# Performance work log

Measured on AMD Instinct MI355X. Metric: run time of the kernel, lower is better.

The kernel has to match this reference:

```python
import jax, jax.numpy as jnp
import numpy as np

N = 50000   # nodes
E = 800000  # edges per layer
D = 128     # feature dim
H = 256     # mlp hidden
O = 3       # output dim


def setup_inputs() -> dict:
    key = jax.random.key(0)
    ks = jax.random.split(key, 16)
    def lin(k, fan_out, fan_in):
        s = 1.0 / np.sqrt(fan_in)
        kw, kb = jax.random.split(k)
        return (jax.random.uniform(kw, (fan_out, fan_in), jnp.float32, -s, s),
                jax.random.uniform(kb, (fan_out,), jnp.float32, -s, s))
    x = jax.random.normal(ks[0], (N, D), jnp.float32)
    edge_idx0 = jax.random.randint(ks[1], (2, E), 0, N, dtype=jnp.int64)
    edge_idx1 = jax.random.randint(ks[2], (2, E), 0, N, dtype=jnp.int64)
    Wl1, bl1 = lin(ks[3], D, D)   # SAGE layer1: lin_l (aggregated neighbors, with bias)
    Wr1, _ = lin(ks[4], D, D)     # SAGE layer1: lin_r (root, no bias)
    Wl2, bl2 = lin(ks[5], D, D)
    Wr2, _ = lin(ks[6], D, D)
    Ws, bs = lin(ks[7], D, D)     # skip_fc
    W1, b1 = lin(ks[8], H, D)     # mlp hidden
    W2, b2 = lin(ks[9], O, H)     # mlp out
    return dict(x=x, edge_idx0=edge_idx0, edge_idx1=edge_idx1,
                Wl1=Wl1, bl1=bl1, Wr1=Wr1, Wl2=Wl2, bl2=bl2, Wr2=Wr2,
                Ws=Ws, bs=bs, W1=W1, b1=b1, W2=W2, b2=b2)


def _sage(x, ei, Wl, bl, Wr):
    # PyG SAGEConv with mean aggregation: out = lin_l(mean_j x_j) + lin_r(x_i)
    src, dst = ei[0], ei[1]
    agg = jax.ops.segment_sum(x[src], dst, num_segments=N)          # [N, D] gather-scatter
    cnt = jax.ops.segment_sum(jnp.ones((ei.shape[1],), x.dtype), dst, num_segments=N)
    agg = agg / jnp.maximum(cnt, 1.0)[:, None]
    return agg @ Wl.T + bl + x @ Wr.T


def reference(x, edge_idx0, edge_idx1, Wl1, bl1, Wr1, Wl2, bl2, Wr2,
              Ws, bs, W1, b1, W2, b2):
    inp = x
    h = _sage(x, edge_idx0, Wl1, bl1, Wr1)
    h = _sage(h, edge_idx1, Wl2, bl2, Wr2)
    h = h + (inp @ Ws.T + bs)            # skip connection
    h = jax.nn.relu(h @ W1.T + b1)       # MLP head
    return h @ W2.T + b2                  # [N, 3]
```

## Files before the change

### kernel.cpp

```cpp
#include <hip/hip_runtime.h>
#include <hip/hip_bf16.h>


#define DD 128
#define SB 8
#define CH 4096
typedef unsigned short u16;
typedef __attribute__((ext_vector_type(8))) short short8;
typedef __attribute__((ext_vector_type(4))) float f32x4;

__device__ inline u16 f2bf(float f) {
    __hip_bfloat16 h = __float2bfloat16(f);
    u16 u;
    __builtin_memcpy(&u, &h, 2);
    return u;
}
__device__ inline unsigned pack2(float lo, float hi) {
    return (unsigned)f2bf(lo) | ((unsigned)f2bf(hi) << 16);
}
__device__ inline float bf_lo(unsigned u) { union { unsigned x; float f; } c; c.x = u << 16; return c.f; }
__device__ inline float bf_hi(unsigned u) { union { unsigned x; float f; } c; c.x = u & 0xffff0000u; return c.f; }

struct CastJobs {
    const float4* src[6];
    uint2* dst[6];
    int qstart[7];
};
__global__ __launch_bounds__(256) void cast_kernel(CastJobs jb) {
    int q = blockIdx.x * 256 + threadIdx.x;
    if (q >= jb.qstart[6]) return;
    int i = 0;
#pragma unroll
    for (int k = 1; k < 6; ++k) if (q >= jb.qstart[k]) i = k;
    int local = q - jb.qstart[i];
    float4 v = jb.src[i][local];
    jb.dst[i][local] = make_uint2(pack2(v.x, v.y), pack2(v.z, v.w));
}

__global__ __launch_bounds__(256) void hist1_kernel(const int* __restrict__ dst0, int* __restrict__ h0,
                                                    const int* __restrict__ dst1, int* __restrict__ h1,
                                                    int e0, int e1, int nb, int P) {
    int arr = blockIdx.y;
    const int* dst = arr ? dst1 : dst0;
    int* hist = arr ? h1 : h0;
    int e = arr ? e1 : e0;
    __shared__ int h[256];
    int t = threadIdx.x;
    h[t] = 0;
    __syncthreads();
    int base = blockIdx.x * CH;
    int hi = min(base + CH, e);
    for (int i = base + t; i < hi; i += 256) atomicAdd(&h[dst[i] >> SB], 1);
    __syncthreads();
    if (t < nb) hist[t * P + blockIdx.x] = h[t];
}

__global__ __launch_bounds__(256) void rowsum_kernel(const int* __restrict__ h0, int* __restrict__ bs0,
                                                     const int* __restrict__ h1, int* __restrict__ bs1,
                                                     int P) {
    int arr = blockIdx.y;
    const int* hist = arr ? h1 : h0;
    int* bs = arr ? bs1 : bs0;
    int b = blockIdx.x;
    __shared__ int s[256];
    int t = threadIdx.x;
    s[t] = (t < P) ? hist[b * P + t] : 0;
    __syncthreads();
    for (int off = 128; off; off >>= 1) {
        if (t < off) s[t] += s[t + off];
        __syncthreads();
    }
    if (t == 0) bs[b] = s[0];
}

__global__ __launch_bounds__(256) void bscan_kernel(const int* __restrict__ bs0, int* __restrict__ bb0, int* __restrict__ rp0, int e0,
                                                    const int* __restrict__ bs1, int* __restrict__ bb1, int* __restrict__ rp1, int e1,
                                                    int nb, int n) {
    int arr = blockIdx.x;
    const int* bsum = arr ? bs1 : bs0;
    int* bb = arr ? bb1 : bb0;
    int* rp = arr ? rp1 : rp0;
    int E = arr ? e1 : e0;
    __shared__ int s[256];
    int t = threadIdx.x;
    int v = (t < nb) ? bsum[t] : 0;
    s[t] = v;
    __syncthreads();
    for (int off = 1; off < 256; off <<= 1) {
        int u = (t >= off) ? s[t - off] : 0;
        __syncthreads();
        s[t] += u;
        __syncthreads();
    }
    if (t < nb) bb[t] = s[t] - v;
    if (t == 0) { bb[nb] = E; rp[n] = E; }
}

__global__ __launch_bounds__(256) void offs_kernel(int* __restrict__ h0, const int* __restrict__ bb0,
                                                   int* __restrict__ h1, const int* __restrict__ bb1,
                                                   int P) {
    int arr = blockIdx.y;
    int* hist = arr ? h1 : h0;
    const int* bb = arr ? bb1 : bb0;
    int b = blockIdx.x;
    __shared__ int s[256];
    int t = threadIdx.x;
    int v = (t < P) ? hist[b * P + t] : 0;
    s[t] = v;
    __syncthreads();
    for (int off = 1; off < 256; off <<= 1) {
        int u = (t >= off) ? s[t - off] : 0;
        __syncthreads();
        s[t] += u;
        __syncthreads();
    }
    if (t < P) hist[b * P + t] = s[t] - v + bb[b];
}

__global__ __launch_bounds__(256) void scatter1_kernel(
    const int* __restrict__ src0, const int* __restrict__ dst0, const int* __restrict__ h0, unsigned* __restrict__ binned0,
    const int* __restrict__ src1, const int* __restrict__ dst1, const int* __restrict__ h1, unsigned* __restrict__ binned1,
    int e0, int e1, int nb, int P) {
    int arr = blockIdx.y;
    const int* src = arr ? src1 : src0;
    const int* dst = arr ? dst1 : dst0;
    const int* hist = arr ? h1 : h0;
    unsigned* binned = arr ? binned1 : binned0;
    int e = arr ? e1 : e0;
    int p = blockIdx.x;
    __shared__ int cnt[256];
    int t = threadIdx.x;
    if (t < nb) cnt[t] = hist[t * P + p];
    __syncthreads();
    int base = p * CH;
    int hi = min(base + CH, e);
    for (int i = base + t; i < hi; i += 256) {
        int d = dst[i];
        int pos = atomicAdd(&cnt[d >> SB], 1);
        binned[pos] = ((unsigned)d << 16) | (unsigned)src[i];
    }
}

__global__ __launch_bounds__(256) void place_kernel(
    const unsigned* __restrict__ binned0, const int* __restrict__ bb0, int* __restrict__ rp0, u16* __restrict__ csr0,
    const unsigned* __restrict__ binned1, const int* __restrict__ bb1, int* __restrict__ rp1, u16* __restrict__ csr1,
    int n, int nb) {
    int arr = blockIdx.y;
    const unsigned* binned = arr ? binned1 : binned0;
    const int* bb = arr ? bb1 : bb0;
    int* rp = arr ? rp1 : rp0;
    u16* csr = arr ? csr1 : csr0;
    int b = blockIdx.x;
    __shared__ int cnt[256];
    __shared__ int s[256];
    int t = threadIdx.x;
    int base = bb[b], end = bb[b + 1];
    cnt[t] = 0;
    __syncthreads();
    for (int i = base + t; i < end; i += 256)
        atomicAdd(&cnt[(binned[i] >> 16) & 255], 1);
    __syncthreads();
    int deg = cnt[t];
    s[t] = deg;
    __syncthreads();
    for (int off = 1; off < 256; off <<= 1) {
        int u = (t >= off) ? s[t - off] : 0;
        __syncthreads();
        s[t] += u;
        __syncthreads();
    }
    int gpos = base + s[t] - deg;
    int node = (b << SB) + t;
    if (node < n) rp[node] = gpos;
    cnt[t] = gpos;
    __syncthreads();
    for (int i = base + t; i < end; i += 256) {
        unsigned pk = binned[i];
        int ld = (pk >> 16) & 255;
        int pos = atomicAdd(&cnt[ld], 1);
        csr[pos] = (u16)(pk & 0xffffu);
    }
}

__global__ __launch_bounds__(256) void agg1_kernel(const unsigned* __restrict__ G1L,
                                                   const unsigned* __restrict__ G1M,
                                                   const u16* __restrict__ csr,
                                                   const int* __restrict__ rp,
                                                   const float* __restrict__ bl1,
                                                   unsigned* __restrict__ h1, int n) {
    int g = (blockIdx.x * 256 + threadIdx.x) >> 6;
    int lane = threadIdx.x & 63;
    if (g >= n) return;
    int start = rp[g], end = rp[g + 1];
    float a0 = 0.f, a1 = 0.f;
    int e = start;
    for (; e + 7 < end; e += 8) {
        int s0 = csr[e],     s1 = csr[e + 1], s2 = csr[e + 2], s3 = csr[e + 3];
        int s4 = csr[e + 4], s5 = csr[e + 5], s6 = csr[e + 6], s7 = csr[e + 7];
        unsigned v0 = G1L[(size_t)s0 * 64 + lane];
        unsigned v1 = G1L[(size_t)s1 * 64 + lane];
        unsigned v2 = G1L[(size_t)s2 * 64 + lane];
        unsigned v3 = G1L[(size_t)s3 * 64 + lane];
        unsigned v4 = G1L[(size_t)s4 * 64 + lane];
        unsigned v5 = G1L[(size_t)s5 * 64 + lane];
        unsigned v6 = G1L[(size_t)s6 * 64 + lane];
        unsigned v7 = G1L[(size_t)s7 * 64 + lane];
        a0 += ((bf_lo(v0) + bf_lo(v1)) + (bf_lo(v2) + bf_lo(v3))) +
              ((bf_lo(v4) + bf_lo(v5)) + (bf_lo(v6) + bf_lo(v7)));
        a1 += ((bf_hi(v0) + bf_hi(v1)) + (bf_hi(v2) + bf_hi(v3))) +
              ((bf_hi(v4) + bf_hi(v5)) + (bf_hi(v6) + bf_hi(v7)));
    }
    for (; e + 3 < end; e += 4) {
        int s0 = csr[e], s1 = csr[e + 1], s2 = csr[e + 2], s3 = csr[e + 3];
        unsigned v0 = G1L[(size_t)s0 * 64 + lane];
        unsigned v1 = G1L[(size_t)s1 * 64 + lane];
        unsigned v2 = G1L[(size_t)s2 * 64 + lane];
        unsigned v3 = G1L[(size_t)s3 * 64 + lane];
        a0 += (bf_lo(v0) + bf_lo(v1)) + (bf_lo(v2) + bf_lo(v3));
        a1 += (bf_hi(v0) + bf_hi(v1)) + (bf_hi(v2) + bf_hi(v3));
    }
    for (; e < end; ++e) {
        unsigned v0 = G1L[(size_t)csr[e] * 64 + lane];
        a0 += bf_lo(v0);
        a1 += bf_hi(v0);
    }
    float sc = 1.0f / (float)max(end - start, 1);
    unsigned m = G1M[(size_t)g * 64 + lane];
    float2 b = ((const float2*)bl1)[lane];
    h1[(size_t)g * 64 + lane] = pack2(a0 * sc + bf_lo(m) + b.x, a1 * sc + bf_hi(m) + b.y);
}

__global__ __launch_bounds__(256) void agg2_kernel(const unsigned* __restrict__ G2L,
                                                   const unsigned* __restrict__ G2R,
                                                   const unsigned* __restrict__ G1R,
                                                   const u16* __restrict__ csr,
                                                   const int* __restrict__ rp,
                                                   const float* __restrict__ bl2,
                                                   const float* __restrict__ bs,
                                                   unsigned* __restrict__ h3, int n) {
    int g = (blockIdx.x * 256 + threadIdx.x) >> 6;
    int lane = threadIdx.x & 63;
    if (g >= n) return;
    int start = rp[g], end = rp[g + 1];
    float a0 = 0.f, a1 = 0.f;
    int e = start;
    for (; e + 7 < end; e += 8) {
        int s0 = csr[e],     s1 = csr[e + 1], s2 = csr[e + 2], s3 = csr[e + 3];
        int s4 = csr[e + 4], s5 = csr[e + 5], s6 = csr[e + 6], s7 = csr[e + 7];
        unsigned v0 = G2L[(size_t)s0 * 64 + lane];
        unsigned v1 = G2L[(size_t)s1 * 64 + lane];
        unsigned v2 = G2L[(size_t)s2 * 64 + lane];
        unsigned v3 = G2L[(size_t)s3 * 64 + lane];
        unsigned v4 = G2L[(size_t)s4 * 64 + lane];
        unsigned v5 = G2L[(size_t)s5 * 64 + lane];
        unsigned v6 = G2L[(size_t)s6 * 64 + lane];
        unsigned v7 = G2L[(size_t)s7 * 64 + lane];
        a0 += ((bf_lo(v0) + bf_lo(v1)) + (bf_lo(v2) + bf_lo(v3))) +
              ((bf_lo(v4) + bf_lo(v5)) + (bf_lo(v6) + bf_lo(v7)));
        a1 += ((bf_hi(v0) + bf_hi(v1)) + (bf_hi(v2) + bf_hi(v3))) +
              ((bf_hi(v4) + bf_hi(v5)) + (bf_hi(v6) + bf_hi(v7)));
    }
    for (; e + 3 < end; e += 4) {
        int s0 = csr[e], s1 = csr[e + 1], s2 = csr[e + 2], s3 = csr[e + 3];
        unsigned v0 = G2L[(size_t)s0 * 64 + lane];
        unsigned v1 = G2L[(size_t)s1 * 64 + lane];
        unsigned v2 = G2L[(size_t)s2 * 64 + lane];
        unsigned v3 = G2L[(size_t)s3 * 64 + lane];
        a0 += (bf_lo(v0) + bf_lo(v1)) + (bf_lo(v2) + bf_lo(v3));
        a1 += (bf_hi(v0) + bf_hi(v1)) + (bf_hi(v2) + bf_hi(v3));
    }
    for (; e < end; ++e) {
        unsigned v0 = G2L[(size_t)csr[e] * 64 + lane];
        a0 += bf_lo(v0);
        a1 += bf_hi(v0);
    }
    float sc = 1.0f / (float)max(end - start, 1);
    unsigned m2 = G2R[(size_t)g * 64 + lane];
    unsigned m1 = G1R[(size_t)g * 64 + lane];
    float2 b = ((const float2*)bl2)[lane];
    float2 s2 = ((const float2*)bs)[lane];
    h3[(size_t)g * 64 + lane] = pack2(a0 * sc + bf_lo(m2) + bf_lo(m1) + b.x + s2.x,
                                      a1 * sc + bf_hi(m2) + bf_hi(m1) + b.y + s2.y);
}

__device__ inline void load_af_f32(const void* Av, int rowA, int half, short8* af) {
    const float4* Arow = (const float4*)Av + (size_t)rowA * 32 + half * 2;
#pragma unroll
    for (int kk = 0; kk < 4; ++kk) {
        float4 a = Arow[kk * 8], b = Arow[kk * 8 + 1];
        uint4 v = make_uint4(pack2(a.x, a.y), pack2(a.z, a.w),
                             pack2(b.x, b.y), pack2(b.z, b.w));
        af[kk] = *(short8*)&v;
    }
}
__device__ inline void load_af_bf16(const void* Av, int rowA, int half, short8* af) {
    const uint4* Arow = (const uint4*)Av + (size_t)rowA * 16 + half;
#pragma unroll
    for (int kk = 0; kk < 4; ++kk) {
        uint4 v = Arow[kk * 4];
        af[kk] = *(short8*)&v;
    }
}

template <bool F32A>
__global__ __launch_bounds__(256) void mfma_gemm(const void* __restrict__ Av,
                                                 const u16* __restrict__ W,
                                                 u16* __restrict__ C, int M) {
    __shared__ u16 Bs[32 * 512];
    const int t = threadIdx.x;
    const int colBase = blockIdx.y * 128;
    u16* Cp = C + (size_t)blockIdx.y * M * 128;
    const int w = t >> 6, lane = t & 63, r = lane & 15, half = lane >> 4;
    const int nTiles = M >> 4;
    const int stride = gridDim.x * 4;
    int tile = blockIdx.x * 4 + w;

    short8 af[4];
    if (tile < nTiles) {
        if (F32A) load_af_f32(Av, (tile << 4) + r, half, af);
        else      load_af_bf16(Av, (tile << 4) + r, half, af);
    }
#pragma unroll
    for (int i = 0; i < 8; ++i) {
        int id = t + 256 * i;
        int nrow = id >> 4, cc = id & 15;
        int f = ((nrow >> 4) << 2) | (cc >> 2);
        int dl = ((cc & 3) << 4) | (nrow & 15);
        *(uint4*)&Bs[(f * 64 + dl) * 8] = ((const uint4*)W)[(size_t)(colBase + nrow) * 16 + cc];
    }
    __syncthreads();
    const u16* bB = &Bs[lane * 8];
    for (; tile < nTiles; tile += stride) {
        int nextTile = tile + stride;
        short8 afn[4];
        if (nextTile < nTiles) {
            if (F32A) load_af_f32(Av, (nextTile << 4) + r, half, afn);
            else      load_af_bf16(Av, (nextTile << 4) + r, half, afn);
        }
        f32x4 acc[8];
#pragma unroll
        for (int i = 0; i < 8; ++i) acc[i] = (f32x4){0.f, 0.f, 0.f, 0.f};
#pragma unroll
        for (int kk = 0; kk < 4; ++kk)
#pragma unroll
            for (int ct = 0; ct < 8; ++ct) {
                short8 bf = *(const short8*)(bB + (ct * 4 + kk) * 512);
                acc[ct] = __builtin_amdgcn_mfma_f32_16x16x32_bf16(af[kk], bf, acc[ct], 0, 0, 0);
            }
#pragma unroll
        for (int ct = 0; ct < 8; ++ct) {
            int col = ct * 16 + r;
#pragma unroll
            for (int reg = 0; reg < 4; ++reg) {
                int row = (tile << 4) + half * 4 + reg;
                Cp[(size_t)row * 128 + col] = f2bf(acc[ct][reg]);
            }
        }
#pragma unroll
        for (int kk = 0; kk < 4; ++kk) af[kk] = afn[kk];
    }
}

__global__ __launch_bounds__(256) void gemm_out_kernel(const u16* __restrict__ h3,
                                                       const u16* __restrict__ W1,
                                                       const float* __restrict__ b1,
                                                       const float* __restrict__ W2,
                                                       const float* __restrict__ b2,
                                                       float* __restrict__ out, int M) {
    __shared__ u16 Bs[64 * 512];
    __shared__ float w2s[3 * 256];
    __shared__ float b1s[256];
    const int t = threadIdx.x;
    const int w = t >> 6, lane = t & 63, r = lane & 15, half = lane >> 4;
    const int nTiles = M >> 4;
    const int stride = gridDim.x * 4;
    int tile = blockIdx.x * 4 + w;

    short8 af[4];
    if (tile < nTiles) load_af_bf16(h3, (tile << 4) + r, half, af);
#pragma unroll
    for (int i = 0; i < 16; ++i) {
        int id = t + 256 * i;
        int nrow = id >> 4, cc = id & 15;
        int f = ((nrow >> 4) << 2) | (cc >> 2);
        int dl = ((cc & 3) << 4) | (nrow & 15);
        *(uint4*)&Bs[(f * 64 + dl) * 8] = ((const uint4*)W1)[(size_t)nrow * 16 + cc];
    }
    for (int i = t; i < 768; i += 256) w2s[i] = W2[i];
    b1s[t] = b1[t];
    __syncthreads();
    const u16* bB = &Bs[lane * 8];
    float c0 = b2[0], c1 = b2[1], c2 = b2[2];
    for (; tile < nTiles; tile += stride) {
        int nextTile = tile + stride;
        short8 afn[4];
        if (nextTile < nTiles) load_af_bf16(h3, (nextTile << 4) + r, half, afn);
        f32x4 acc[16];
#pragma unroll
        for (int i = 0; i < 16; ++i) acc[i] = (f32x4){0.f, 0.f, 0.f, 0.f};
#pragma unroll
        for (int kk = 0; kk < 4; ++kk)
#pragma unroll
            for (int ct = 0; ct < 16; ++ct) {
                short8 bf = *(const short8*)(bB + (ct * 4 + kk) * 512);
                acc[ct] = __builtin_amdgcn_mfma_f32_16x16x32_bf16(af[kk], bf, acc[ct], 0, 0, 0);
            }
        float p[4][3] = {{0.f, 0.f, 0.f}, {0.f, 0.f, 0.f}, {0.f, 0.f, 0.f}, {0.f, 0.f, 0.f}};
#pragma unroll
        for (int ct = 0; ct < 16; ++ct) {
            int col = ct * 16 + r;
            float bv = b1s[col];
            float w0 = w2s[col], w1 = w2s[256 + col], w2v = w2s[512 + col];
#pragma unroll
            for (int reg = 0; reg < 4; ++reg) {
                float h4 = fmaxf(acc[ct][reg] + bv, 0.f);
                p[reg][0] += h4 * w0;
                p[reg][1] += h4 * w1;
                p[reg][2] += h4 * w2v;
            }
        }
#pragma unroll
        for (int m = 1; m < 16; m <<= 1)
#pragma unroll
            for (int reg = 0; reg < 4; ++reg) {
                p[reg][0] += __shfl_xor(p[reg][0], m);
                p[reg][1] += __shfl_xor(p[reg][1], m);
                p[reg][2] += __shfl_xor(p[reg][2], m);
            }
        if (r == 0) {
#pragma unroll
            for (int reg = 0; reg < 4; ++reg) {
                int row = (tile << 4) + half * 4 + reg;
                out[(size_t)row * 3 + 0] = p[reg][0] + c0;
                out[(size_t)row * 3 + 1] = p[reg][1] + c1;
                out[(size_t)row * 3 + 2] = p[reg][2] + c2;
            }
        }
#pragma unroll
        for (int kk = 0; kk < 4; ++kk) af[kk] = afn[kk];
    }
}

extern "C" void kernel_launch(void* const* d_in, const int* in_sizes, int n_in,
                              void* d_out, int out_size, void* d_ws, size_t ws_size,
                              hipStream_t stream) {
    const float* x   = (const float*)d_in[0];
    const int*   ei0 = (const int*)d_in[1];
    const int*   ei1 = (const int*)d_in[2];
    const float* Wl1 = (const float*)d_in[3];
    const float* bl1 = (const float*)d_in[4];
    const float* Wr1 = (const float*)d_in[5];
    const float* Wl2 = (const float*)d_in[6];
    const float* bl2 = (const float*)d_in[7];
    const float* Wr2 = (const float*)d_in[8];
    const float* Wsk = (const float*)d_in[9];
    const float* bsk = (const float*)d_in[10];
    const float* W1  = (const float*)d_in[11];
    const float* b1  = (const float*)d_in[12];
    const float* W2  = (const float*)d_in[13];
    const float* b2  = (const float*)d_in[14];
    float* out = (float*)d_out;

    const int N  = in_sizes[0] / DD;
    const int E0 = in_sizes[1] / 2;
    const int E1 = in_sizes[2] / 2;
    const int H  = in_sizes[12];

    const int* src0 = ei0;      const int* dst0 = ei0 + E0;
    const int* src1 = ei1;      const int* dst1 = ei1 + E1;

    const int nb   = (N + 255) >> SB;
    const int Emax = (E0 > E1) ? E0 : E1;
    const int P    = (Emax + CH - 1) / CH;

    char* wp = (char*)d_ws;
    auto carve = [&](size_t bytes) { char* p = wp; wp += (bytes + 255) & ~(size_t)255; return p; };
    u16* G1   = (u16*)carve((size_t)3 * N * DD * 2);
    u16* G2   = (u16*)carve((size_t)2 * N * DD * 2);
    u16* h1h  = (u16*)carve((size_t)N * DD * 2);
    u16* h3h  = (u16*)carve((size_t)N * DD * 2);
    u16* wc1  = (u16*)carve((size_t)384 * DD * 2);
    u16* wc2  = (u16*)carve((size_t)256 * DD * 2);
    u16* w1h  = (u16*)carve((size_t)H * DD * 2);
    int* rp0  = (int*)carve((size_t)(N + 1) * 4);
    int* rp1  = (int*)carve((size_t)(N + 1) * 4);
    u16* csr0 = (u16*)carve((size_t)E0 * 2);
    u16* csr1 = (u16*)carve((size_t)E1 * 2);
    unsigned* binned0 = (unsigned*)carve((size_t)E0 * 4);
    unsigned* binned1 = (unsigned*)carve((size_t)E1 * 4);
    int* hist1_0 = (int*)carve((size_t)nb * P * 4);
    int* hist1_1 = (int*)carve((size_t)nb * P * 4);
    int* bsum0 = (int*)carve((size_t)nb * 4);
    int* bsum1 = (int*)carve((size_t)nb * 4);
    int* bb0 = (int*)carve((size_t)(nb + 1) * 4);
    int* bb1 = (int*)carve((size_t)(nb + 1) * 4);

    const u16* G1L = G1;
    const u16* G1M = G1 + (size_t)N * DD;
    const u16* G1R = G1 + (size_t)2 * N * DD;
    const u16* G2L = G2;
    const u16* G2R = G2 + (size_t)N * DD;

    CastJobs jb;
    const float* srcs[6] = {Wl1, Wr1, Wsk, Wl2, Wr2, W1};
    u16* dsts[6] = {wc1, wc1 + 128 * DD, wc1 + 256 * DD, wc2, wc2 + 128 * DD, w1h};
    int  cnts[6] = {DD * DD, DD * DD, DD * DD, DD * DD, DD * DD, H * DD};
    int q = 0;
    for (int i = 0; i < 6; ++i) {
        jb.src[i] = (const float4*)srcs[i];
        jb.dst[i] = (uint2*)dsts[i];
        jb.qstart[i] = q;
        q += cnts[i] / 4;
    }
    jb.qstart[6] = q;

    const int gAgg = (N * 64 + 255) / 256;

    cast_kernel<<<(q + 255) / 256, 256, 0, stream>>>(jb);
    hist1_kernel<<<dim3(P, 2), 256, 0, stream>>>(dst0, hist1_0, dst1, hist1_1, E0, E1, nb, P);
    rowsum_kernel<<<dim3(nb, 2), 256, 0, stream>>>(hist1_0, bsum0, hist1_1, bsum1, P);
    bscan_kernel<<<2, 256, 0, stream>>>(bsum0, bb0, rp0, E0, bsum1, bb1, rp1, E1, nb, N);
    offs_kernel<<<dim3(nb, 2), 256, 0, stream>>>(hist1_0, bb0, hist1_1, bb1, P);
    scatter1_kernel<<<dim3(P, 2), 256, 0, stream>>>(src0, dst0, hist1_0, binned0,
                                                    src1, dst1, hist1_1, binned1, E0, E1, nb, P);
    place_kernel<<<dim3(nb, 2), 256, 0, stream>>>(binned0, bb0, rp0, csr0,
                                                  binned1, bb1, rp1, csr1, N, nb);

    mfma_gemm<true><<<dim3(320, 3), 256, 0, stream>>>(x, wc1, G1, N);
    agg1_kernel<<<gAgg, 256, 0, stream>>>((const unsigned*)G1L, (const unsigned*)G1M,
                                          csr0, rp0, bl1, (unsigned*)h1h, N);
    mfma_gemm<false><<<dim3(320, 2), 256, 0, stream>>>(h1h, wc2, G2, N);
    agg2_kernel<<<gAgg, 256, 0, stream>>>((const unsigned*)G2L, (const unsigned*)G2R,
                                          (const unsigned*)G1R, csr1, rp1, bl2, bsk,
                                          (unsigned*)h3h, N);
    gemm_out_kernel<<<512, 256, 0, stream>>>(h3h, w1h, b1, W2, b2, out, N);
}
```

Measured before the change: 261.4 us.

## Chunk neighbor features by column slice per XCD and fuse weight cast into GEMMs

The GEMM now writes the lin_l projection in four 32-column chunks stored contiguously per chunk. The aggregation kernels map block IDs so each pair of XCDs gathers only one chunk, keeping each XCD's gather working set (about 3.2MB) small enough to stay in its L2. Separately, the standalone weight-cast kernel is removed, and the GEMMs convert fp32 weights to bf16 while loading them into LDS. This trades one launch for redundant per-block conversion work. Each node's gather now uses 16 lanes, so more edge-index reads are repeated across chunks.

After: 285.9 us. +9.3%, slower.

```diff
diff --git a/kernel.cpp b/kernel.cpp
--- a/kernel.cpp
+++ b/kernel.cpp
@@ -20,22 +20,6 @@
 }
 __device__ inline float bf_lo(unsigned u) { union { unsigned x; float f; } c; c.x = u << 16; return c.f; }
 __device__ inline float bf_hi(unsigned u) { union { unsigned x; float f; } c; c.x = u & 0xffff0000u; return c.f; }
-
-struct CastJobs {
-    const float4* src[6];
-    uint2* dst[6];
-    int qstart[7];
-};
-__global__ __launch_bounds__(256) void cast_kernel(CastJobs jb) {
-    int q = blockIdx.x * 256 + threadIdx.x;
-    if (q >= jb.qstart[6]) return;
-    int i = 0;
-#pragma unroll
-    for (int k = 1; k < 6; ++k) if (q >= jb.qstart[k]) i = k;
-    int local = q - jb.qstart[i];
-    float4 v = jb.src[i][local];
-    jb.dst[i][local] = make_uint2(pack2(v.x, v.y), pack2(v.z, v.w));
-}
 
 __global__ __launch_bounds__(256) void hist1_kernel(const int* __restrict__ dst0, int* __restrict__ h0,
                                                     const int* __restrict__ dst1, int* __restrict__ h1,
@@ -182,55 +166,52 @@
     }
 }
 
-__global__ __launch_bounds__(256) void agg1_kernel(const unsigned* __restrict__ G1L,
+__global__ __launch_bounds__(256) void agg1_kernel(const unsigned* __restrict__ G1Lc,
                                                    const unsigned* __restrict__ G1M,
                                                    const u16* __restrict__ csr,
                                                    const int* __restrict__ rp,
                                                    const float* __restrict__ bl1,
                                                    unsigned* __restrict__ h1, int n) {
-    int g = (blockIdx.x * 256 + threadIdx.x) >> 6;
-    int lane = threadIdx.x & 63;
+    int xcd = blockIdx.x & 7;
+    int chunk = xcd >> 1;
+    int nodeBlock = (blockIdx.x >> 3) * 2 + (xcd & 1);
+    int w = threadIdx.x >> 6, lane = threadIdx.x & 63;
+    int g = nodeBlock * 16 + w * 4 + (lane >> 4);
+    int c = lane & 15;
     if (g >= n) return;
+    const unsigned* base = G1Lc + (size_t)chunk * n * 16;
     int start = rp[g], end = rp[g + 1];
     float a0 = 0.f, a1 = 0.f;
     int e = start;
     for (; e + 7 < end; e += 8) {
         int s0 = csr[e],     s1 = csr[e + 1], s2 = csr[e + 2], s3 = csr[e + 3];
         int s4 = csr[e + 4], s5 = csr[e + 5], s6 = csr[e + 6], s7 = csr[e + 7];
-        unsigned v0 = G1L[(size_t)s0 * 64 + lane];
-        unsigned v1 = G1L[(size_t)s1 * 64 + lane];
-        unsigned v2 = G1L[(size_t)s2 * 64 + lane];
-        unsigned v3 = G1L[(size_t)s3 * 64 + lane];
-        unsigned v4 = G1L[(size_t)s4 * 64 + lane];
-        unsigned v5 = G1L[(size_t)s5 * 64 + lane];
-        unsigned v6 = G1L[(size_t)s6 * 64 + lane];
-        unsigned v7 = G1L[(size_t)s7 * 64 + lane];
+        unsigned v0 = base[(size_t)s0 * 16 + c];
+        unsigned v1 = base[(size_t)s1 * 16 + c];
+        unsigned v2 = base[(size_t)s2 * 16 + c];
+        unsigned v3 = base[(size_t)s3 * 16 + c];
+        unsigned v4 = base[(size_t)s4 * 16 + c];
+        unsigned v5 = base[(size_t)s5 * 16 + c];
+        unsigned v6 = base[(size_t)s6 * 16 + c];
+        unsigned v7 = base[(size_t)s7 * 16 + c];
         a0 += ((bf_lo(v0) + bf_lo(v1)) + (bf_lo(v2) + bf_lo(v3))) +
               ((bf_lo(v4) + bf_lo(v5)) + (bf_lo(v6) + bf_lo(v7)));
         a1 += ((bf_hi(v0) + bf_hi(v1)) + (bf_hi(v2) + bf_hi(v3))) +
               ((bf_hi(v4) + bf_hi(v5)) + (bf_hi(v6) + bf_hi(v7)));
     }
-    for (; e + 3 < end; e += 4) {
-        int s0 = csr[e], s1 = csr[e + 1], s2 = csr[e + 2], s3 = csr[e + 3];
-        unsigned v0 = G1L[(size_t)s0 * 64 + lane];
-        unsigned v1 = G1L[(size_t)s1 * 64 + lane];
-        unsigned v2 = G1L[(size_t)s2 * 64 + lane];
-        unsigned v3 = G1L[(size_t)s3 * 64 + lane];
-        a0 += (bf_lo(v0) + bf_lo(v1)) + (bf_lo(v2) + bf_lo(v3));
-        a1 += (bf_hi(v0) + bf_hi(v1)) + (bf_hi(v2) + bf_hi(v3));
-    }
     for (; e < end; ++e) {
-        unsigned v0 = G1L[(size_t)csr[e] * 64 + lane];
+        unsigned v0 = base[(size_t)csr[e] * 16 + c];
         a0 += bf_lo(v0);
         a1 += bf_hi(v0);
     }
     float sc = 1.0f / (float)max(end - start, 1);
-    unsigned m = G1M[(size_t)g * 64 + lane];
-    float2 b = ((const float2*)bl1)[lane];
-    h1[(size_t)g * 64 + lane] = pack2(a0 * sc + bf_lo(m) + b.x, a1 * sc + bf_hi(m) + b.y);
-}
-
-__global__ __launch_bounds__(256) void agg2_kernel(const unsigned* __restrict__ G2L,
+    int col = chunk * 16 + c;
+    unsigned m = G1M[(size_t)g * 64 + col];
+    float2 b = ((const float2*)bl1)[col];
+    h1[(size_t)g * 64 + col] = pack2(a0 * sc + bf_lo(m) + b.x, a1 * sc + bf_hi(m) + b.y);
+}
+
+__global__ __launch_bounds__(256) void agg2_kernel(const unsigned* __restrict__ G2Lc,
                                                    const unsigned* __restrict__ G2R,
                                                    const unsigned* __restrict__ G1R,
                                                    const u16* __restrict__ csr,
@@ -238,49 +219,46 @@
                                                    const float* __restrict__ bl2,
                                                    const float* __restrict__ bs,
                                                    unsigned* __restrict__ h3, int n) {
-    int g = (blockIdx.x * 256 + threadIdx.x) >> 6;
-    int lane = threadIdx.x & 63;
+    int xcd = blockIdx.x & 7;
+    int chunk = xcd >> 1;
+    int nodeBlock = (blockIdx.x >> 3) * 2 + (xcd & 1);
+    int w = threadIdx.x >> 6, lane = threadIdx.x & 63;
+    int g = nodeBlock * 16 + w * 4 + (lane >> 4);
+    int c = lane & 15;
     if (g >= n) return;
+    const unsigned* base = G2Lc + (size_t)chunk * n * 16;
     int start = rp[g], end = rp[g + 1];
     float a0 = 0.f, a1 = 0.f;
     int e = start;
     for (; e + 7 < end; e += 8) {
         int s0 = csr[e],     s1 = csr[e + 1], s2 = csr[e + 2], s3 = csr[e + 3];
         int s4 = csr[e + 4], s5 = csr[e + 5], s6 = csr[e + 6], s7 = csr[e + 7];
-        unsigned v0 = G2L[(size_t)s0 * 64 + lane];
-        unsigned v1 = G2L[(size_t)s1 * 64 + lane];
-        unsigned v2 = G2L[(size_t)s2 * 64 + lane];
-        unsigned v3 = G2L[(size_t)s3 * 64 + lane];
-        unsigned v4 = G2L[(size_t)s4 * 64 + lane];
-        unsigned v5 = G2L[(size_t)s5 * 64 + lane];
-        unsigned v6 = G2L[(size_t)s6 * 64 + lane];
-        unsigned v7 = G2L[(size_t)s7 * 64 + lane];
+        unsigned v0 = base[(size_t)s0 * 16 + c];
+        unsigned v1 = base[(size_t)s1 * 16 + c];
+        unsigned v2 = base[(size_t)s2 * 16 + c];
+        unsigned v3 = base[(size_t)s3 * 16 + c];
+        unsigned v4 = base[(size_t)s4 * 16 + c];
+        unsigned v5 = base[(size_t)s5 * 16 + c];
+        unsigned v6 = base[(size_t)s6 * 16 + c];
+        unsigned v7 = base[(size_t)s7 * 16 + c];
         a0 += ((bf_lo(v0) + bf_lo(v1)) + (bf_lo(v2) + bf_lo(v3))) +
               ((bf_lo(v4) + bf_lo(v5)) + (bf_lo(v6) + bf_lo(v7)));
         a1 += ((bf_hi(v0) + bf_hi(v1)) + (bf_hi(v2) + bf_hi(v3))) +
               ((bf_hi(v4) + bf_hi(v5)) + (bf_hi(v6) + bf_hi(v7)));
     }
-    for (; e + 3 < end; e += 4) {
-        int s0 = csr[e], s1 = csr[e + 1], s2 = csr[e + 2], s3 = csr[e + 3];
-        unsigned v0 = G2L[(size_t)s0 * 64 + lane];
-        unsigned v1 = G2L[(size_t)s1 * 64 + lane];
-        unsigned v2 = G2L[(size_t)s2 * 64 + lane];
-        unsigned v3 = G2L[(size_t)s3 * 64 + lane];
-        a0 += (bf_lo(v0) + bf_lo(v1)) + (bf_lo(v2) + bf_lo(v3));
-        a1 += (bf_hi(v0) + bf_hi(v1)) + (bf_hi(v2) + bf_hi(v3));
-    }
     for (; e < end; ++e) {
-        unsigned v0 = G2L[(size_t)csr[e] * 64 + lane];
+        unsigned v0 = base[(size_t)csr[e] * 16 + c];
         a0 += bf_lo(v0);
         a1 += bf_hi(v0);
     }
     float sc = 1.0f / (float)max(end - start, 1);
-    unsigned m2 = G2R[(size_t)g * 64 + lane];
-    unsigned m1 = G1R[(size_t)g * 64 + lane];
-    float2 b = ((const float2*)bl2)[lane];
-    float2 s2 = ((const float2*)bs)[lane];
-    h3[(size_t)g * 64 + lane] = pack2(a0 * sc + bf_lo(m2) + bf_lo(m1) + b.x + s2.x,
-                                      a1 * sc + bf_hi(m2) + bf_hi(m1) + b.y + s2.y);
+    int col = chunk * 16 + c;
+    unsigned m2 = G2R[(size_t)g * 64 + col];
+    unsigned m1 = G1R[(size_t)g * 64 + col];
+    float2 b = ((const float2*)bl2)[col];
+    float2 s2 = ((const float2*)bs)[col];
+    h3[(size_t)g * 64 + col] = pack2(a0 * sc + bf_lo(m2) + bf_lo(m1) + b.x + s2.x,
+                                     a1 * sc + bf_hi(m2) + bf_hi(m1) + b.y + s2.y);
 }
 
 __device__ inline void load_af_f32(const void* Av, int rowA, int half, short8* af) {
@@ -302,13 +280,15 @@
     }
 }
 
-template <bool F32A>
+template <bool F32A, bool CHUNK0>
 __global__ __launch_bounds__(256) void mfma_gemm(const void* __restrict__ Av,
-                                                 const u16* __restrict__ W,
+                                                 const float* __restrict__ Wa,
+                                                 const float* __restrict__ Wb,
+                                                 const float* __restrict__ Wc,
                                                  u16* __restrict__ C, int M) {
     __shared__ u16 Bs[32 * 512];
     const int t = threadIdx.x;
-    const int colBase = blockIdx.y * 128;
+    const float* Wsel = (blockIdx.y == 0) ? Wa : (blockIdx.y == 1 ? Wb : Wc);
     u16* Cp = C + (size_t)blockIdx.y * M * 128;
     const int w = t >> 6, lane = t & 63, r = lane & 15, half = lane >> 4;
     const int nTiles = M >> 4;
@@ -326,7 +306,11 @@
         int nrow = id >> 4, cc = id & 15;
         int f = ((nrow >> 4) << 2) | (cc >> 2);
         int dl = ((cc & 3) << 4) | (nrow & 15);
-        *(uint4*)&Bs[(f * 64 + dl) * 8] = ((const uint4*)W)[(size_t)(colBase + nrow) * 16 + cc];
+        const float4* wr = (const float4*)&Wsel[(size_t)nrow * 128 + cc * 8];
+        float4 a = wr[0], b = wr[1];
+        uint4 v = make_uint4(pack2(a.x, a.y), pack2(a.z, a.w),
+                             pack2(b.x, b.y), pack2(b.z, b.w));
+        *(uint4*)&Bs[(f * 64 + dl) * 8] = v;
     }
     __syncthreads();
     const u16* bB = &Bs[lane * 8];
@@ -347,13 +331,26 @@
                 short8 bf = *(const short8*)(bB + (ct * 4 + kk) * 512);
                 acc[ct] = __builtin_amdgcn_mfma_f32_16x16x32_bf16(af[kk], bf, acc[ct], 0, 0, 0);
             }
-#pragma unroll
-        for (int ct = 0; ct < 8; ++ct) {
-            int col = ct * 16 + r;
-#pragma unroll
-            for (int reg = 0; reg < 4; ++reg) {
-                int row = (tile << 4) + half * 4 + reg;
-                Cp[(size_t)row * 128 + col] = f2bf(acc[ct][reg]);
+        if (CHUNK0 && blockIdx.y == 0) {
+#pragma unroll
+            for (int ct = 0; ct < 8; ++ct) {
+                int chunk = ct >> 1;
+                int cc = ((ct & 1) << 4) + r;
+#pragma unroll
+                for (int reg = 0; reg < 4; ++reg) {
+                    int row = (tile << 4) + half * 4 + reg;
+                    Cp[(size_t)chunk * M * 32 + (size_t)row * 32 + cc] = f2bf(acc[ct][reg]);
+                }
+            }
+        } else {
+#pragma unroll
+            for (int ct = 0; ct < 8; ++ct) {
+                int col = ct * 16 + r;
+#pragma unroll
+                for (int reg = 0; reg < 4; ++reg) {
+                    int row = (tile << 4) + half * 4 + reg;
+                    Cp[(size_t)row * 128 + col] = f2bf(acc[ct][reg]);
+                }
             }
         }
 #pragma unroll
@@ -362,7 +359,7 @@
 }
 
 __global__ __launch_bounds__(256) void gemm_out_kernel(const u16* __restrict__ h3,
-                                                       const u16* __restrict__ W1,
+                                                       const float* __restrict__ W1,
                                                        const float* __restrict__ b1,
                                                        const float* __restrict__ W2,
                                                        const float* __restrict__ b2,
@@ -384,7 +381,11 @@
         int nrow = id >> 4, cc = id & 15;
         int f = ((nrow >> 4) << 2) | (cc >> 2);
         int dl = ((cc & 3) << 4) | (nrow & 15);
-        *(uint4*)&Bs[(f * 64 + dl) * 8] = ((const uint4*)W1)[(size_t)nrow * 16 + cc];
+        const float4* wr = (const float4*)&W1[(size_t)nrow * 128 + cc * 8];
+        float4 a = wr[0], b = wr[1];
+        uint4 v = make_uint4(pack2(a.x, a.y), pack2(a.z, a.w),
+                             pack2(b.x, b.y), pack2(b.z, b.w));
+        *(uint4*)&Bs[(f * 64 + dl) * 8] = v;
     }
     for (int i = t; i < 768; i += 256) w2s[i] = W2[i];
     b1s[t] = b1[t];
@@ -479,9 +480,6 @@
     u16* G2   = (u16*)carve((size_t)2 * N * DD * 2);
     u16* h1h  = (u16*)carve((size_t)N * DD * 2);
     u16* h3h  = (u16*)carve((size_t)N * DD * 2);
-    u16* wc1  = (u16*)carve((size_t)384 * DD * 2);
-    u16* wc2  = (u16*)carve((size_t)256 * DD * 2);
-    u16* w1h  = (u16*)carve((size_t)H * DD * 2);
     int* rp0  = (int*)carve((size_t)(N + 1) * 4);
     int* rp1  = (int*)carve((size_t)(N + 1) * 4);
     u16* csr0 = (u16*)carve((size_t)E0 * 2);
@@ -495,28 +493,13 @@
     int* bb0 = (int*)carve((size_t)(nb + 1) * 4);
     int* bb1 = (int*)carve((size_t)(nb + 1) * 4);
 
-    const u16* G1L = G1;
     const u16* G1M = G1 + (size_t)N * DD;
     const u16* G1R = G1 + (size_t)2 * N * DD;
-    const u16* G2L = G2;
     const u16* G2R = G2 + (size_t)N * DD;
 
-    CastJobs jb;
-    const float* srcs[6] = {Wl1, Wr1, Wsk, Wl2, Wr2, W1};
-    u16* dsts[6] = {wc1, wc1 + 128 * DD, wc1 + 256 * DD, wc2, wc2 + 128 * DD, w1h};
-    int  cnts[6] = {DD * DD, DD * DD, DD * DD, DD * DD, DD * DD, H * DD};
-    int q = 0;
-    for (int i = 0; i < 6; ++i) {
-        jb.src[i] = (const float4*)srcs[i];
-        jb.dst[i] = (uint2*)dsts[i];
-        jb.qstart[i] = q;
-        q += cnts[i] / 4;
-    }
-    jb.qstart[6] = q;
-
-    const int gAgg = (N * 64 + 255) / 256;
-
-    cast_kernel<<<(q + 255) / 256, 256, 0, stream>>>(jb);
+    const int nodeBlocks = (N + 15) / 16;
+    const int gAgg = 8 * ((nodeBlocks + 1) / 2);
+
     hist1_kernel<<<dim3(P, 2), 256, 0, stream>>>(dst0, hist1_0, dst1, hist1_1, E0, E1, nb, P);
     rowsum_kernel<<<dim3(nb, 2), 256, 0, stream>>>(hist1_0, bsum0, hist1_1, bsum1, P);
     bscan_kernel<<<2, 256, 0, stream>>>(bsum0, bb0, rp0, E0, bsum1, bb1, rp1, E1, nb, N);
@@ -526,12 +509,12 @@
     place_kernel<<<dim3(nb, 2), 256, 0, stream>>>(binned0, bb0, rp0, csr0,
                                                   binned1, bb1, rp1, csr1, N, nb);
 
-    mfma_gemm<true><<<dim3(320, 3), 256, 0, stream>>>(x, wc1, G1, N);
-    agg1_kernel<<<gAgg, 256, 0, stream>>>((const unsigned*)G1L, (const unsigned*)G1M,
+    mfma_gemm<true, true><<<dim3(320, 3), 256, 0, stream>>>(x, Wl1, Wr1, Wsk, G1, N);
+    agg1_kernel<<<gAgg, 256, 0, stream>>>((const unsigned*)G1, (const unsigned*)G1M,
                                           csr0, rp0, bl1, (unsigned*)h1h, N);
-    mfma_gemm<false><<<dim3(320, 2), 256, 0, stream>>>(h1h, wc2, G2, N);
-    agg2_kernel<<<gAgg, 256, 0, stream>>>((const unsigned*)G2L, (const unsigned*)G2R,
+    mfma_gemm<false, true><<<dim3(320, 2), 256, 0, stream>>>(h1h, Wl2, Wr2, nullptr, G2, N);
+    agg2_kernel<<<gAgg, 256, 0, stream>>>((const unsigned*)G2, (const unsigned*)G2R,
                                           (const unsigned*)G1R, csr1, rp1, bl2, bsk,
                                           (unsigned*)h3h, N);
-    gemm_out_kernel<<<512, 256, 0, stream>>>(h3h, w1h, b1, W2, b2, out, N);
-}
+    gemm_out_kernel<<<512, 256, 0, stream>>>(h3h, W1, b1, W2, b2, out, N);
+}
```
